# Kernel tuning notes

Hardware: AMD Instinct MI355X
Metric: run time of the kernel (lower is better)

## Reference

```python
import math
import jax, jax.numpy as jnp
import numpy as np

B, S, D, H = 4, 1024, 512, 8
DK = D // H


def lin(x, W, b):
    # torch nn.Linear: y = x @ W.T + b, W: [out, in]
    return jnp.einsum('...i,oi->...o', x, W) + b


def layer_norm(x, scale, bias, eps=1e-5):
    m = jnp.mean(x, axis=-1, keepdims=True)
    v = jnp.var(x, axis=-1, keepdims=True)
    return (x - m) / jnp.sqrt(v + eps) * scale + bias


def mha(q_in, k_in, v_in, Wq, bq, Wk, bk, Wv, bv, Wo, bo, gammas, mask, zero_pad):
    b, s, _ = q_in.shape
    q = lin(q_in, Wq, bq).reshape(b, s, H, DK).transpose(0, 2, 1, 3)  # bhsd
    k = lin(k_in, Wk, bk).reshape(b, s, H, DK).transpose(0, 2, 1, 3)
    v = lin(v_in, Wv, bv).reshape(b, s, H, DK).transpose(0, 2, 1, 3)
    scores = jnp.einsum('bhid,bhjd->bhij', q, k) / math.sqrt(DK)
    # no-grad distance-decay branch
    s_ = jnp.where(mask, scores, jnp.float32(-1e32))
    s_ = jax.nn.softmax(s_, axis=-1) * mask
    distcum = jnp.cumsum(s_, axis=-1)
    disttotal = jnp.sum(s_, axis=-1, keepdims=True)
    idx = jnp.arange(s)
    pos = jnp.abs(idx[None, :] - idx[:, None]).astype(jnp.float32)[None, None]  # |i-j|
    dist = jax.lax.stop_gradient(jnp.sqrt(jnp.clip((disttotal - distcum) * pos, 0.0, None)))
    gamma = -jax.nn.softplus(gammas)[None]  # [1,h,1,1]
    total_effect = jnp.clip(jnp.exp(dist * gamma), 1e-5, 1e5)
    scores = scores * total_effect
    # NOTE: original code calls scores.masked_fill(...) without assignment (no-op);
    # faithfully NOT re-masking before this softmax.
    att = jax.nn.softmax(scores, axis=-1)
    if zero_pad:
        att = att.at[:, :, 0, :].set(0.0)
    out = jnp.einsum('bhij,bhjd->bhid', att, v).transpose(0, 2, 1, 3).reshape(b, s, D)
    return lin(out, Wo, bo)


def setup_inputs() -> dict:
    key = jax.random.key(0)
    ks = jax.random.split(key, 32)
    ki = iter(range(32))

    def w(shape, scale=0.02):
        return jax.random.normal(ks[next(ki)], shape, jnp.float32) * scale

    inp = {
        'q_emb': jax.random.normal(ks[next(ki)], (B, S, D), jnp.float32),
        'qa_emb': jax.random.normal(ks[next(ki)], (B, S, D), jnp.float32),
    }
    for blk in (1, 2, 3):
        inp[f'Wq{blk}'] = w((D, D)); inp[f'bq{blk}'] = jnp.zeros((D,), jnp.float32)
        if blk == 3:
            inp['Wk3'] = w((D, D)); inp['bk3'] = jnp.zeros((D,), jnp.float32)
        inp[f'Wv{blk}'] = w((D, D)); inp[f'bv{blk}'] = jnp.zeros((D,), jnp.float32)
        inp[f'Wo{blk}'] = w((D, D)); inp[f'bo{blk}'] = jnp.zeros((D,), jnp.float32)
        inp[f'g{blk}'] = w((H, 1, 1), 0.5)
        inp[f'ls{blk}'] = jnp.ones((D,), jnp.float32)
        inp[f'lb{blk}'] = jnp.zeros((D,), jnp.float32)
    inp['know'] = jax.random.uniform(ks[next(ki)], (1, 1, D), jnp.float32, -1.0, 1.0)
    inp['Wlk'] = w((D, DK)); inp['b_lk'] = jnp.zeros((D,), jnp.float32)
    inp['Wlv'] = w((D, DK)); inp['b_lv'] = jnp.zeros((D,), jnp.float32)
    return inp


def reference(q_emb, qa_emb,
              Wq1, bq1, Wv1, bv1, Wo1, bo1, g1, ls1, lb1,
              Wq2, bq2, Wv2, bv2, Wo2, bo2, g2, ls2, lb2,
              Wq3, bq3, Wk3, bk3, Wv3, bv3, Wo3, bo3, g3, ls3, lb3,
              know, Wlk, b_lk, Wlv, b_lv):
    b, s, d = q_emb.shape
    ones = jnp.ones((s, s), dtype=bool)
    mask_peek = jnp.tril(ones, k=0)[None, None]   # peek_cur=True
    mask_nopeek = jnp.tril(ones, k=-1)[None, None]  # peek_cur=False

    # block1 / block2 share k and q projections (kq_same=True)
    hq = layer_norm(q_emb + mha(q_emb, q_emb, q_emb, Wq1, bq1, Wq1, bq1,
                                Wv1, bv1, Wo1, bo1, g1, mask_peek, False), ls1, lb1)
    ha = layer_norm(qa_emb + mha(qa_emb, qa_emb, qa_emb, Wq2, bq2, Wq2, bq2,
                                 Wv2, bv2, Wo2, bo2, g2, mask_peek, False), ls2, lb2)
    query = jnp.broadcast_to(know, (b, s, d))
    h = layer_norm(query + mha(query, hq, ha, Wq3, bq3, Wk3, bk3,
                               Wv3, bv3, Wo3, bo3, g3, mask_nopeek, True), ls3, lb3)

    # small multi-head combine
    key_t = jax.nn.sigmoid(lin(query.reshape(b, s, H, DK), Wlk, b_lk))  # [b,s,h,d]
    val_t = jax.nn.sigmoid(lin(h.reshape(b, s, H, DK), Wlv, b_lv))     # [b,s,h,d]
    beta = jnp.einsum('bshd,bsd->bsh', key_t, q_emb)
    alpha = jax.nn.softmax(beta, axis=-1)
    out = jnp.einsum('bsh,bshd->bsd', alpha, val_t)
    return out
```

## Files before the change

kernel.cpp:

```cpp
#include <hip/hip_runtime.h>
#include <math.h>

#define BB 4
#define S 1024
#define D 512
#define H 8
#define DKH 64

#define ATT_LD 1032
#define KS_LD  66

typedef __attribute__((ext_vector_type(8))) short bf16x8;
typedef __attribute__((ext_vector_type(4))) float f32x4;

__device__ __forceinline__ unsigned short f2bf(float f){
  unsigned int u = __float_as_uint(f);
  u += 0x7FFFu + ((u >> 16) & 1u);
  return (unsigned short)(u >> 16);
}
__device__ __forceinline__ float bf2f(unsigned int v){
  return __uint_as_float(v << 16);
}
__device__ __forceinline__ f32x4 MFMA(bf16x8 a, bf16x8 b, f32x4 c){
  return __builtin_amdgcn_mfma_f32_16x16x32_bf16(a, b, c, 0, 0, 0);
}
__device__ __forceinline__ void gl_lds16(const void* g, void* l){
  __builtin_amdgcn_global_load_lds(
      (const __attribute__((address_space(1))) void*)g,
      (__attribute__((address_space(3))) void*)l, 16, 0, 0);
}

__device__ __forceinline__ float blk_sum(float* r, int t, float v){
  r[t] = v; __syncthreads();
  for (int s = 128; s > 0; s >>= 1){
    if (t < s) r[t] += r[t + s];
    __syncthreads();
  }
  float res = r[0]; __syncthreads();
  return res;
}

struct GemmJobs {
  const unsigned short* A[4];
  const unsigned short* W[4];
  const float* bias[4];
  void* C[4];
};
template<int OUTBF>
__global__ __launch_bounds__(256) void mfma_gemm_b(GemmJobs jb)
{
  __shared__ __align__(16) short As[128][32];
  __shared__ __align__(16) short Ws[128][32];
  const int t = threadIdx.x;
  const int z = blockIdx.z;
  const int n0 = blockIdx.x * 128, m0 = blockIdx.y * 128;
  const unsigned short* A = jb.A[z];
  const unsigned short* W = jb.W[z];
  const float* bias = jb.bias[z];
  const int w = t >> 6, lane = t & 63;
  const int wm = (w >> 1) << 6, wn = (w & 1) << 6;
  const int lm = lane & 15, q = lane >> 4;
  const int r = t >> 2, cc = (t & 3) << 3;
  char* ldsA = ((char*)&As[0][0]) + w * 1024;
  char* ldsW = ((char*)&Ws[0][0]) + w * 1024;
  f32x4 acc[4][4];
  #pragma unroll
  for (int a_ = 0; a_ < 4; a_++)
    #pragma unroll
    for (int b_ = 0; b_ < 4; b_++)
      acc[a_][b_] = (f32x4){0.f, 0.f, 0.f, 0.f};
  for (int k0 = 0; k0 < D; k0 += 32){
    gl_lds16(&A[(size_t)(m0 + r)      * D + k0 + cc], ldsA);
    gl_lds16(&A[(size_t)(m0 + r + 64) * D + k0 + cc], ldsA + 4096);
    gl_lds16(&W[(size_t)(n0 + r)      * D + k0 + cc], ldsW);
    gl_lds16(&W[(size_t)(n0 + r + 64) * D + k0 + cc], ldsW + 4096);
    __syncthreads();
    bf16x8 af[4], bf[4];
    #pragma unroll
    for (int mt = 0; mt < 4; mt++) af[mt] = *(const bf16x8*)&As[wm + mt*16 + lm][q*8];
    #pragma unroll
    for (int nt = 0; nt < 4; nt++) bf[nt] = *(const bf16x8*)&Ws[wn + nt*16 + lm][q*8];
    #pragma unroll
    for (int mt = 0; mt < 4; mt++)
      #pragma unroll
      for (int nt = 0; nt < 4; nt++)
        acc[mt][nt] = MFMA(af[mt], bf[nt], acc[mt][nt]);
    __syncthreads();
  }
  #pragma unroll
  for (int nt = 0; nt < 4; nt++){
    const int n = n0 + wn + nt*16 + lm;
    const float bs = bias[n];
    #pragma unroll
    for (int mt = 0; mt < 4; mt++){
      const int mb = m0 + wm + mt*16 + (q << 2);
      f32x4 c = acc[mt][nt];
      #pragma unroll
      for (int rr = 0; rr < 4; rr++){
        float vv = c[rr] + bs;
        if (OUTBF)
          ((unsigned short*)jb.C[z])[(size_t)(mb + rr) * D + n] = f2bf(vv);
        else
          ((float*)jb.C[z])[(size_t)(mb + rr) * D + n] = vv;
      }
    }
  }
}

struct VTArgs { const unsigned short* v[2]; unsigned short* vt[2]; };
__global__ __launch_bounds__(256) void vt_kernel(VTArgs a)
{
  __shared__ unsigned short tile[64 * KS_LD];
  const int z = blockIdx.z, bh = blockIdx.y, b = bh >> 3, h = bh & 7;
  const int j0 = blockIdx.x * 64;
  const int t = threadIdx.x;
  const unsigned short* vp = a.v[z];
  unsigned short* vtp = a.vt[z] + (size_t)bh * 64 * S;
  #pragma unroll
  for (int p = 0; p < 2; p++){
    int lin = t + p * 256, row = lin >> 3, c8 = (lin & 7) << 3;
    *(uint4*)&tile[row * KS_LD + c8] =
      *(const uint4*)&vp[((size_t)b * S + j0 + row) * D + h * DKH + c8];
  }
  __syncthreads();
  #pragma unroll
  for (int p = 0; p < 2; p++){
    int lin = t + p * 256, d = lin >> 3, c8 = (lin & 7) << 3;
    unsigned short tmp[8];
    #pragma unroll
    for (int jx = 0; jx < 8; jx++) tmp[jx] = tile[(c8 + jx) * KS_LD + d];
    *(uint4*)&vtp[(size_t)d * S + j0 + c8] = *(const uint4*)tmp;
  }
}

struct FAArgs {
  const unsigned short* qk[2];
  const unsigned short* vt[2];
  unsigned short* ctx[2];
  const float* g[2];
  const float* c3;
  int diag, zero_pad;
};
template<int C3>
__global__ __launch_bounds__(256) void fused_attn(FAArgs a)
{
  __shared__ __align__(16) unsigned short att[32 * ATT_LD];
  __shared__ __align__(16) unsigned short Ks[64 * KS_LD];
  const int t = threadIdx.x;
  const int z = blockIdx.z;
  const int bh = blockIdx.y, b = bh >> 3, h = bh & 7;
  const int i0 = blockIdx.x * 32;
  const int w = t >> 6, lane = t & 63, lm = lane & 15, q = lane >> 4;
  const unsigned short* qkp = a.qk[z];
  const unsigned short* vtp = a.vt[z] + (size_t)bh * 64 * S;
  unsigned short* ctxp = a.ctx[z];
  const int r0 = t >> 3, c8 = (t & 7) << 3;
  float gm;
  { float gv = a.g[z][h]; gm = -((gv > 20.f) ? gv : log1pf(expf(gv))); }

  if (!C3){
    bf16x8 af[2][2];
    #pragma unroll
    for (int mt = 0; mt < 2; mt++)
      #pragma unroll
      for (int kft = 0; kft < 2; kft++)
        af[mt][kft] = *(const bf16x8*)
          &qkp[((size_t)b * S + i0 + mt*16 + lm) * D + h * DKH + kft*32 + q*8];
    uint4 k0v = *(const uint4*)&qkp[((size_t)b * S + r0)      * D + h * DKH + c8];
    uint4 k1v = *(const uint4*)&qkp[((size_t)b * S + r0 + 32) * D + h * DKH + c8];
    for (int jc = 0; jc < S; jc += 64){
      *(uint4*)&Ks[r0 * KS_LD + c8]        = k0v;
      *(uint4*)&Ks[(r0 + 32) * KS_LD + c8] = k1v;
      __syncthreads();
      if (jc + 64 < S){
        k0v = *(const uint4*)&qkp[((size_t)b * S + jc + 64 + r0)      * D + h * DKH + c8];
        k1v = *(const uint4*)&qkp[((size_t)b * S + jc + 64 + r0 + 32) * D + h * DKH + c8];
      }
      bf16x8 bv0 = *(const bf16x8*)&Ks[(w*16 + lm) * KS_LD + q*8];
      bf16x8 bv1 = *(const bf16x8*)&Ks[(w*16 + lm) * KS_LD + 32 + q*8];
      #pragma unroll
      for (int mt = 0; mt < 2; mt++){
        f32x4 acc = (f32x4){0.f, 0.f, 0.f, 0.f};
        acc = MFMA(af[mt][0], bv0, acc);
        acc = MFMA(af[mt][1], bv1, acc);
        #pragma unroll
        for (int rr = 0; rr < 4; rr++)
          att[(mt*16 + q*4 + rr) * ATT_LD + jc + w*16 + lm] = f2bf(acc[rr] * 0.125f);
      }
      __syncthreads();
    }
  }

  uint4 v0 = *(const uint4*)&vtp[(size_t)r0 * S + c8];
  uint4 v1 = *(const uint4*)&vtp[(size_t)(r0 + 32) * S + c8];

  const int jA0 = lane * 8, jB0 = 512 + lane * 8;
  for (int rloc = 0; rloc < 8; rloc++){
    const int i = i0 + w*8 + rloc;
    unsigned short* rowp = &att[(w*8 + rloc) * ATT_LD];
    if (C3 && a.zero_pad && i == 0){
      uint4 zz = make_uint4(0u,0u,0u,0u);
      *(uint4*)&rowp[jA0] = zz;
      *(uint4*)&rowp[jB0] = zz;
      continue;
    }
    float c[16];
    if (C3){
      const float* c3p = a.c3 + ((size_t)b * H + h) * S;
      #pragma unroll
      for (int sg = 0; sg < 2; sg++)
        #pragma unroll
        for (int p4 = 0; p4 < 2; p4++){
          float4 x = *(const float4*)&c3p[sg*512 + lane*8 + p4*4];
          c[sg*8+p4*4+0] = x.x; c[sg*8+p4*4+1] = x.y;
          c[sg*8+p4*4+2] = x.z; c[sg*8+p4*4+3] = x.w;
        }
    } else {
      #pragma unroll
      for (int sg = 0; sg < 2; sg++){
        uint4 u = *(const uint4*)&rowp[sg*512 + lane*8];
        unsigned int uu[4] = {u.x, u.y, u.z, u.w};
        #pragma unroll
        for (int mel = 0; mel < 4; mel++){
          c[sg*8 + mel*2]     = bf2f(uu[mel] & 0xffffu);
          c[sg*8 + mel*2 + 1] = bf2f(uu[mel] >> 16);
        }
      }
    }
    const int jmax = i + a.diag;
    float pl[16];
    float runA = 0.f, runB = 0.f;
    #pragma unroll
    for (int k = 0; k < 8; k++){
      float e = (jA0 + k <= jmax) ? __expf(c[k]) : 0.f;
      runA += e; pl[k] = runA;
    }
    #pragma unroll
    for (int k = 0; k < 8; k++){
      float e = (jB0 + k <= jmax) ? __expf(c[8+k]) : 0.f;
      runB += e; pl[8+k] = runB;
    }
    float sA = runA, sB = runB;
    #pragma unroll
    for (int off = 1; off < 64; off <<= 1){
      float uA = __shfl_up(sA, off, 64);
      float uB = __shfl_up(sB, off, 64);
      if (lane >= off){ sA += uA; sB += uB; }
    }
    const float TA = __shfl(sA, 63, 64);
    const float T  = TA + __shfl(sB, 63, 64);
    const float inv1 = 1.f / T;
    const float cbaseA = (T - (sA - runA)) * inv1;
    const float cbaseB = (T - (TA + sB - runB)) * inv1;
    const float fiA = (float)(i - jA0);
    const float fiB = (float)(i - jB0);
    float ls2 = 0.f;
    #pragma unroll
    for (int k = 0; k < 8; k++){
      float remn = fmaf(-pl[k], inv1, cbaseA);
      float pos  = fabsf(fiA - (float)k);
      float dist = sqrtf(fmaxf(remn * pos, 0.f));
      float eff  = fmaxf(__expf(gm * dist), 1e-5f);
      float pp   = __expf(c[k] * eff);
      ls2 += pp; pl[k] = pp;
    }
    #pragma unroll
    for (int k = 0; k < 8; k++){
      float remn = fmaf(-pl[8+k], inv1, cbaseB);
      float pos  = fabsf(fiB - (float)k);
      float dist = sqrtf(fmaxf(remn * pos, 0.f));
      float eff  = fmaxf(__expf(gm * dist), 1e-5f);
      float pp   = __expf(c[8+k] * eff);
      ls2 += pp; pl[8+k] = pp;
    }
    #pragma unroll
    for (int off = 1; off < 64; off <<= 1) ls2 += __shfl_xor(ls2, off, 64);
    const float inv2 = 1.f / ls2;
    #pragma unroll
    for (int sg = 0; sg < 2; sg++){
      unsigned int ou[4];
      #pragma unroll
      for (int mel = 0; mel < 4; mel++){
        unsigned int lo = f2bf(pl[sg*8 + 2*mel]     * inv2);
        unsigned int hi = f2bf(pl[sg*8 + 2*mel + 1] * inv2);
        ou[mel] = lo | (hi << 16);
      }
      *(uint4*)&rowp[sg*512 + lane*8] = make_uint4(ou[0], ou[1], ou[2], ou[3]);
    }
  }
  __syncthreads();

  const int mloc = w & 1, nh = w >> 1;
  f32x4 acc0 = (f32x4){0.f,0.f,0.f,0.f};
  f32x4 acc1 = (f32x4){0.f,0.f,0.f,0.f};
  for (int kc = 0; kc < S; kc += 64){
    *(uint4*)&Ks[r0 * KS_LD + c8]        = v0;
    *(uint4*)&Ks[(r0 + 32) * KS_LD + c8] = v1;
    __syncthreads();
    if (kc + 64 < S){
      v0 = *(const uint4*)&vtp[(size_t)r0 * S + kc + 64 + c8];
      v1 = *(const uint4*)&vtp[(size_t)(r0 + 32) * S + kc + 64 + c8];
    }
    #pragma unroll
    for (int kft = 0; kft < 2; kft++){
      bf16x8 afv = *(const bf16x8*)&att[(mloc*16 + lm) * ATT_LD + kc + kft*32 + q*8];
      bf16x8 b0 = *(const bf16x8*)&Ks[((nh*2 + 0)*16 + lm) * KS_LD + kft*32 + q*8];
      bf16x8 b1 = *(const bf16x8*)&Ks[((nh*2 + 1)*16 + lm) * KS_LD + kft*32 + q*8];
      acc0 = MFMA(afv, b0, acc0);
      acc1 = MFMA(afv, b1, acc1);
    }
    __syncthreads();
  }
  #pragma unroll
  for (int nt2 = 0; nt2 < 2; nt2++){
    f32x4 acc = nt2 ? acc1 : acc0;
    const int d = (nh*2 + nt2)*16 + lm;
    #pragma unroll
    for (int rr = 0; rr < 4; rr++){
      const int row = i0 + mloc*16 + q*4 + rr;
      ctxp[((size_t)b * S + row) * D + h * DKH + d] = f2bf(acc[rr]);
    }
  }
}

__global__ __launch_bounds__(256) void ln_residual(
    const float* __restrict__ resid, const float* __restrict__ y,
    const float* __restrict__ ls, const float* __restrict__ lb,
    unsigned short* __restrict__ out, int bcast)
{
  const int r = blockIdx.x, t = threadIdx.x;
  __shared__ float red[256];
  const size_t base = (size_t)r * D;
  float r0 = bcast ? resid[t]       : resid[base + t];
  float r1 = bcast ? resid[t + 256] : resid[base + t + 256];
  float x0 = r0 + y[base + t];
  float x1 = r1 + y[base + t + 256];
  float mean = blk_sum(red, t, x0 + x1) * (1.0f / 512.0f);
  float d0 = x0 - mean, d1 = x1 - mean;
  float var = blk_sum(red, t, d0*d0 + d1*d1) * (1.0f / 512.0f);
  float inv = rsqrtf(var + 1e-5f);
  out[base + t]       = f2bf(d0 * inv * ls[t]       + lb[t]);
  out[base + t + 256] = f2bf(d1 * inv * ls[t + 256] + lb[t + 256]);
}

struct CvtJobs {
  const float* s[12];
  unsigned short* d[12];
  int n[12];
};
__global__ __launch_bounds__(256) void cvt_all(CvtJobs jb){
  const int z = blockIdx.y;
  const int n = jb.n[z];
  const float* s = jb.s[z];
  unsigned short* d = jb.d[z];
  for (int idx = blockIdx.x * 256 + threadIdx.x; idx < n; idx += gridDim.x * 256)
    d[idx] = f2bf(s[idx]);
}

__global__ __launch_bounds__(256) void qvec3_kernel(
    const float* __restrict__ know, const float* __restrict__ Wq3,
    const float* __restrict__ bq3, float* __restrict__ q3)
{
  int n = blockIdx.x * 256 + threadIdx.x;
  float acc = 0.f;
  for (int d = 0; d < 512; d++) acc += know[d] * Wq3[(size_t)n * 512 + d];
  q3[n] = acc + bq3[n];
}

__global__ __launch_bounds__(256) void keyt_kernel(
    const float* __restrict__ know, const float* __restrict__ Wlk,
    const float* __restrict__ blk_, float* __restrict__ keyt)
{
  int idx = blockIdx.x * 256 + threadIdx.x;
  int h = idx >> 9, n = idx & 511;
  float acc = 0.f;
  for (int i = 0; i < 64; i++) acc += know[h * 64 + i] * Wlk[(size_t)n * 64 + i];
  keyt[idx] = 1.f / (1.f + __expf(-(acc + blk_[n])));
}

__global__ __launch_bounds__(256) void scores3_kernel(
    const float* __restrict__ q3, const unsigned short* __restrict__ k3,
    float* __restrict__ c3)
{
  int idx = blockIdx.x * 256 + threadIdx.x;
  int j  = idx & (S - 1);
  int bh = idx >> 10;
  int h  = bh & 7, b = bh >> 3;
  const unsigned short* kp = k3 + ((size_t)b * S + j) * D + h * DKH;
  const float* qp = q3 + h * DKH;
  float acc = 0.f;
  #pragma unroll
  for (int d8 = 0; d8 < 64; d8 += 8){
    uint4 u = *(const uint4*)&kp[d8];
    unsigned int uu[4] = {u.x, u.y, u.z, u.w};
    #pragma unroll
    for (int mel = 0; mel < 4; mel++){
      acc += qp[d8 + 2*mel]     * bf2f(uu[mel] & 0xffffu);
      acc += qp[d8 + 2*mel + 1] * bf2f(uu[mel] >> 16);
    }
  }
  c3[idx] = acc * 0.125f;
}

__global__ __launch_bounds__(256) void alphas_kernel(
    const float* __restrict__ keyt, const float* __restrict__ q_emb,
    float* __restrict__ alpha)
{
  const int row = blockIdx.x * 4 + (threadIdx.x >> 6);
  const int l = threadIdx.x & 63;
  const int h = l >> 3, sub = l & 7;
  const float* qr = q_emb + (size_t)row * D;
  const float* kt = keyt + h * D;
  float p = 0.f;
  for (int d = sub; d < D; d += 8) p += kt[d] * qr[d];
  p += __shfl_xor(p, 1, 64);
  p += __shfl_xor(p, 2, 64);
  p += __shfl_xor(p, 4, 64);
  float m = p;
  m = fmaxf(m, __shfl_xor(m, 8, 64));
  m = fmaxf(m, __shfl_xor(m, 16, 64));
  m = fmaxf(m, __shfl_xor(m, 32, 64));
  float e = __expf(p - m);
  float ssum = e;
  ssum += __shfl_xor(ssum, 8, 64);
  ssum += __shfl_xor(ssum, 16, 64);
  ssum += __shfl_xor(ssum, 32, 64);
  if (sub == 0) alpha[(size_t)row * H + h] = e / ssum;
}

__global__ __launch_bounds__(256) void val_fused(
    const unsigned short* __restrict__ Ah,
    const unsigned short* __restrict__ Wv,
    const float* __restrict__ blv,
    const float* __restrict__ alpha,
    float* __restrict__ out)
{
  __shared__ __align__(16) short As[128][32];
  __shared__ __align__(16) short Ws[128][32];
  __shared__ float als[128];
  const int t = threadIdx.x;
  const int n0 = blockIdx.x * 128, m0 = blockIdx.y * 128;
  if (t < 128) als[t] = alpha[m0 + t];
  const int w = t >> 6, lane = t & 63;
  const int wm = (w >> 1) << 6, wn = (w & 1) << 6;
  const int lm = lane & 15, q = lane >> 4;
  const int r = t >> 2, cc = (t & 3) << 3;
  f32x4 acc[4][4];
  #pragma unroll
  for (int a_ = 0; a_ < 4; a_++)
    #pragma unroll
    for (int b_ = 0; b_ < 4; b_++)
      acc[a_][b_] = (f32x4){0.f, 0.f, 0.f, 0.f};
  for (int k0 = 0; k0 < 64; k0 += 32){
    *(uint4*)&As[r][cc]      = *(const uint4*)&Ah[(size_t)(m0 + r) * 64 + k0 + cc];
    *(uint4*)&As[r + 64][cc] = *(const uint4*)&Ah[(size_t)(m0 + r + 64) * 64 + k0 + cc];
    *(uint4*)&Ws[r][cc]      = *(const uint4*)&Wv[(size_t)(n0 + r) * 64 + k0 + cc];
    *(uint4*)&Ws[r + 64][cc] = *(const uint4*)&Wv[(size_t)(n0 + r + 64) * 64 + k0 + cc];
    __syncthreads();
    bf16x8 af[4], bf[4];
    #pragma unroll
    for (int mt = 0; mt < 4; mt++) af[mt] = *(const bf16x8*)&As[wm + mt*16 + lm][q*8];
    #pragma unroll
    for (int nt = 0; nt < 4; nt++) bf[nt] = *(const bf16x8*)&Ws[wn + nt*16 + lm][q*8];
    #pragma unroll
    for (int mt = 0; mt < 4; mt++)
      #pragma unroll
      for (int nt = 0; nt < 4; nt++)
        acc[mt][nt] = MFMA(af[mt], bf[nt], acc[mt][nt]);
    __syncthreads();
  }
  #pragma unroll
  for (int nt = 0; nt < 4; nt++){
    const int n = n0 + wn + nt*16 + lm;
    const float bs = blv[n];
    #pragma unroll
    for (int mt = 0; mt < 4; mt++){
      const int mb = m0 + wm + mt*16;
      f32x4 c = acc[mt][nt];
      float part = 0.f;
      #pragma unroll
      for (int rr = 0; rr < 4; rr++){
        const int ml = (mb - m0) + (q << 2) + rr;
        float sg = 1.f / (1.f + __expf(-(c[rr] + bs)));
        part += als[ml] * sg;
      }
      part += __shfl_xor(part, 16, 64);
      if ((q & 1) == 0){
        const int srow = (mb >> 3) + (q >> 1);
        out[(size_t)srow * D + n] = part;
      }
    }
  }
}

extern "C" void kernel_launch(void* const* d_in, const int* in_sizes, int n_in,
                              void* d_out, int out_size, void* d_ws, size_t ws_size,
                              hipStream_t stream) {
  const float* q_emb  = (const float*)d_in[0];
  const float* qa_emb = (const float*)d_in[1];
  const float* Wq1 = (const float*)d_in[2],  *bq1 = (const float*)d_in[3];
  const float* Wv1 = (const float*)d_in[4],  *bv1 = (const float*)d_in[5];
  const float* Wo1 = (const float*)d_in[6],  *bo1 = (const float*)d_in[7];
  const float* g1  = (const float*)d_in[8],  *ls1 = (const float*)d_in[9],  *lb1 = (const float*)d_in[10];
  const float* Wq2 = (const float*)d_in[11], *bq2 = (const float*)d_in[12];
  const float* Wv2 = (const float*)d_in[13], *bv2 = (const float*)d_in[14];
  const float* Wo2 = (const float*)d_in[15], *bo2 = (const float*)d_in[16];
  const float* g2  = (const float*)d_in[17], *ls2 = (const float*)d_in[18], *lb2 = (const float*)d_in[19];
  const float* Wq3 = (const float*)d_in[20], *bq3 = (const float*)d_in[21];
  const float* Wk3 = (const float*)d_in[22], *bk3 = (const float*)d_in[23];
  const float* Wv3 = (const float*)d_in[24], *bv3 = (const float*)d_in[25];
  const float* Wo3 = (const float*)d_in[26], *bo3 = (const float*)d_in[27];
  const float* g3  = (const float*)d_in[28], *ls3 = (const float*)d_in[29], *lb3 = (const float*)d_in[30];
  const float* know = (const float*)d_in[31];
  const float* Wlk  = (const float*)d_in[32], *b_lk = (const float*)d_in[33];
  const float* Wlv  = (const float*)d_in[34], *b_lv = (const float*)d_in[35];
  float* outp = (float*)d_out;

  const size_t NSD = (size_t)BB * S * D;
  unsigned short* p = (unsigned short*)d_ws;
  unsigned short* qk1b = p; p += NSD;
  unsigned short* v1b  = p; p += NSD;
  unsigned short* qk2b = p; p += NSD;
  unsigned short* v2b  = p; p += NSD;
  unsigned short* k3b  = p; p += NSD;
  unsigned short* v3b  = p; p += NSD;
  unsigned short* ctx1b= p; p += NSD;
  unsigned short* ctx2b= p; p += NSD;
  unsigned short* ctx3b= p; p += NSD;
  unsigned short* xqb  = p; p += NSD;
  unsigned short* xab  = p; p += NSD;
  unsigned short* hqb  = p; p += NSD;
  unsigned short* hab  = p; p += NSD;
  unsigned short* hfb  = p; p += NSD;
  unsigned short* vt1  = p; p += NSD;
  unsigned short* vt2  = p; p += NSD;
  unsigned short* vt3  = p; p += NSD;
  unsigned short* wb   = p; p += (size_t)9 * D * D;
  unsigned short* wlvb = p; p += (size_t)D * DKH;
  float* yv0   = (float*)p;
  float* yv1   = yv0 + NSD;
  float* q3    = yv1 + NSD;
  float* keyt  = q3 + 512;
  float* c3    = keyt + 4096;
  float* alpha = c3 + (size_t)BB * H * S;

  unsigned short* Wq1b = wb + 0*(size_t)D*D;
  unsigned short* Wv1b = wb + 1*(size_t)D*D;
  unsigned short* Wo1b = wb + 2*(size_t)D*D;
  unsigned short* Wq2b = wb + 3*(size_t)D*D;
  unsigned short* Wv2b = wb + 4*(size_t)D*D;
  unsigned short* Wo2b = wb + 5*(size_t)D*D;
  unsigned short* Wk3b = wb + 6*(size_t)D*D;
  unsigned short* Wv3b = wb + 7*(size_t)D*D;
  unsigned short* Wo3b = wb + 8*(size_t)D*D;

  CvtJobs jb;
  jb.s[0] = q_emb;  jb.d[0] = xqb;  jb.n[0] = (int)NSD;
  jb.s[1] = qa_emb; jb.d[1] = xab;  jb.n[1] = (int)NSD;
  jb.s[2] = Wq1; jb.d[2] = Wq1b; jb.n[2] = D*D;
  jb.s[3] = Wv1; jb.d[3] = Wv1b; jb.n[3] = D*D;
  jb.s[4] = Wo1; jb.d[4] = Wo1b; jb.n[4] = D*D;
  jb.s[5] = Wq2; jb.d[5] = Wq2b; jb.n[5] = D*D;
  jb.s[6] = Wv2; jb.d[6] = Wv2b; jb.n[6] = D*D;
  jb.s[7] = Wo2; jb.d[7] = Wo2b; jb.n[7] = D*D;
  jb.s[8] = Wk3; jb.d[8] = Wk3b; jb.n[8] = D*D;
  jb.s[9] = Wv3; jb.d[9] = Wv3b; jb.n[9] = D*D;
  jb.s[10] = Wo3; jb.d[10] = Wo3b; jb.n[10] = D*D;
  jb.s[11] = Wlv; jb.d[11] = wlvb; jb.n[11] = D*DKH;
  cvt_all<<<dim3(256, 12), 256, 0, stream>>>(jb);

  {
    GemmJobs g;
    g.A[0]=xqb; g.W[0]=Wq1b; g.bias[0]=bq1; g.C[0]=qk1b;
    g.A[1]=xqb; g.W[1]=Wv1b; g.bias[1]=bv1; g.C[1]=v1b;
    g.A[2]=xab; g.W[2]=Wq2b; g.bias[2]=bq2; g.C[2]=qk2b;
    g.A[3]=xab; g.W[3]=Wv2b; g.bias[3]=bv2; g.C[3]=v2b;
    mfma_gemm_b<1><<<dim3(4, 32, 4), 256, 0, stream>>>(g);
  }
  { VTArgs a; a.v[0]=v1b; a.v[1]=v2b; a.vt[0]=vt1; a.vt[1]=vt2;
    vt_kernel<<<dim3(16, 32, 2), 256, 0, stream>>>(a); }
  { FAArgs a;
    a.qk[0]=qk1b; a.qk[1]=qk2b; a.vt[0]=vt1; a.vt[1]=vt2;
    a.ctx[0]=ctx1b; a.ctx[1]=ctx2b; a.g[0]=g1; a.g[1]=g2;
    a.c3=nullptr; a.diag=0; a.zero_pad=0;
    fused_attn<0><<<dim3(32, 32, 2), 256, 0, stream>>>(a); }
  {
    GemmJobs g;
    g.A[0]=ctx1b; g.W[0]=Wo1b; g.bias[0]=bo1; g.C[0]=yv0;
    g.A[1]=ctx2b; g.W[1]=Wo2b; g.bias[1]=bo2; g.C[1]=yv1;
    g.A[2]=ctx1b; g.W[2]=Wo1b; g.bias[2]=bo1; g.C[2]=yv0;
    g.A[3]=ctx1b; g.W[3]=Wo1b; g.bias[3]=bo1; g.C[3]=yv0;
    mfma_gemm_b<0><<<dim3(4, 32, 2), 256, 0, stream>>>(g);
  }
  ln_residual<<<BB*S, 256, 0, stream>>>(q_emb,  yv0, ls1, lb1, hqb, 0);
  ln_residual<<<BB*S, 256, 0, stream>>>(qa_emb, yv1, ls2, lb2, hab, 0);

  qvec3_kernel<<<2, 256, 0, stream>>>(know, Wq3, bq3, q3);
  {
    GemmJobs g;
    g.A[0]=hqb; g.W[0]=Wk3b; g.bias[0]=bk3; g.C[0]=k3b;
    g.A[1]=hab; g.W[1]=Wv3b; g.bias[1]=bv3; g.C[1]=v3b;
    g.A[2]=hqb; g.W[2]=Wk3b; g.bias[2]=bk3; g.C[2]=k3b;
    g.A[3]=hqb; g.W[3]=Wk3b; g.bias[3]=bk3; g.C[3]=k3b;
    mfma_gemm_b<1><<<dim3(4, 32, 2), 256, 0, stream>>>(g);
  }
  { VTArgs a; a.v[0]=v3b; a.v[1]=v3b; a.vt[0]=vt3; a.vt[1]=vt3;
    vt_kernel<<<dim3(16, 32, 1), 256, 0, stream>>>(a); }
  scores3_kernel<<<128, 256, 0, stream>>>(q3, k3b, c3);
  { FAArgs a;
    a.qk[0]=k3b; a.qk[1]=k3b; a.vt[0]=vt3; a.vt[1]=vt3;
    a.ctx[0]=ctx3b; a.ctx[1]=ctx3b; a.g[0]=g3; a.g[1]=g3;
    a.c3=c3; a.diag=-1; a.zero_pad=1;
    fused_attn<1><<<dim3(32, 32, 1), 256, 0, stream>>>(a); }
  {
    GemmJobs g;
    g.A[0]=ctx3b; g.W[0]=Wo3b; g.bias[0]=bo3; g.C[0]=yv0;
    g.A[1]=ctx3b; g.W[1]=Wo3b; g.bias[1]=bo3; g.C[1]=yv0;
    g.A[2]=ctx3b; g.W[2]=Wo3b; g.bias[2]=bo3; g.C[2]=yv0;
    g.A[3]=ctx3b; g.W[3]=Wo3b; g.bias[3]=bo3; g.C[3]=yv0;
    mfma_gemm_b<0><<<dim3(4, 32, 1), 256, 0, stream>>>(g);
  }
  ln_residual<<<BB*S, 256, 0, stream>>>(know, yv0, ls3, lb3, hfb, 1);

  keyt_kernel<<<16, 256, 0, stream>>>(know, Wlk, b_lk, keyt);
  alphas_kernel<<<1024, 256, 0, stream>>>(keyt, q_emb, alpha);
  val_fused<<<dim3(4, 256), 256, 0, stream>>>(hfb, wlvb, b_lv, alpha, outp);
}
```

Before: 482.4 us.

## Halve attention row tile, drop K/V LDS staging, use exp2, wave-parallel qvec3

The fused attention kernel now handles 16 query rows per block instead of 32, which doubles the grid and halves the LDS score buffer so more blocks fit per CU. K and V^T fragments are read straight from global memory rather than staged through shared memory, removing the per-chunk __syncthreads barriers. The softmax and decay exponentials are rewritten in base 2 with pre-scaled LOG2E inputs. The qvec3 GEMV now uses one wave per output with vectorized loads and a shuffle reduction instead of one thread per output. The trade-off is more redundant global and L2 traffic for K/V, since each block loads them without LDS reuse.

```diff
diff --git a/kernel.cpp b/kernel.cpp
--- a/kernel.cpp
+++ b/kernel.cpp
@@ -8,7 +8,7 @@
 #define DKH 64
 
 #define ATT_LD 1032
-#define KS_LD  66
+#define LOG2E 1.4426950408889634f
 
 typedef __attribute__((ext_vector_type(8))) short bf16x8;
 typedef __attribute__((ext_vector_type(4))) float f32x4;
@@ -107,6 +107,7 @@
   }
 }
 
+#define KS_LD 66
 struct VTArgs { const unsigned short* v[2]; unsigned short* vt[2]; };
 __global__ __launch_bounds__(256) void vt_kernel(VTArgs a)
 {
@@ -144,60 +145,41 @@
 template<int C3>
 __global__ __launch_bounds__(256) void fused_attn(FAArgs a)
 {
-  __shared__ __align__(16) unsigned short att[32 * ATT_LD];
-  __shared__ __align__(16) unsigned short Ks[64 * KS_LD];
+  __shared__ __align__(16) unsigned short att[16 * ATT_LD];
   const int t = threadIdx.x;
   const int z = blockIdx.z;
   const int bh = blockIdx.y, b = bh >> 3, h = bh & 7;
-  const int i0 = blockIdx.x * 32;
+  const int i0 = blockIdx.x * 16;
   const int w = t >> 6, lane = t & 63, lm = lane & 15, q = lane >> 4;
   const unsigned short* qkp = a.qk[z];
   const unsigned short* vtp = a.vt[z] + (size_t)bh * 64 * S;
   unsigned short* ctxp = a.ctx[z];
-  const int r0 = t >> 3, c8 = (t & 7) << 3;
-  float gm;
-  { float gv = a.g[z][h]; gm = -((gv > 20.f) ? gv : log1pf(expf(gv))); }
+  float gm2;
+  { float gv = a.g[z][h];
+    gm2 = -((gv > 20.f) ? gv : log1pf(expf(gv))) * LOG2E; }
 
   if (!C3){
-    bf16x8 af[2][2];
-    #pragma unroll
-    for (int mt = 0; mt < 2; mt++)
-      #pragma unroll
-      for (int kft = 0; kft < 2; kft++)
-        af[mt][kft] = *(const bf16x8*)
-          &qkp[((size_t)b * S + i0 + mt*16 + lm) * D + h * DKH + kft*32 + q*8];
-    uint4 k0v = *(const uint4*)&qkp[((size_t)b * S + r0)      * D + h * DKH + c8];
-    uint4 k1v = *(const uint4*)&qkp[((size_t)b * S + r0 + 32) * D + h * DKH + c8];
+    bf16x8 af0 = *(const bf16x8*)&qkp[((size_t)b * S + i0 + lm) * D + h * DKH + q*8];
+    bf16x8 af1 = *(const bf16x8*)&qkp[((size_t)b * S + i0 + lm) * D + h * DKH + 32 + q*8];
     for (int jc = 0; jc < S; jc += 64){
-      *(uint4*)&Ks[r0 * KS_LD + c8]        = k0v;
-      *(uint4*)&Ks[(r0 + 32) * KS_LD + c8] = k1v;
-      __syncthreads();
-      if (jc + 64 < S){
-        k0v = *(const uint4*)&qkp[((size_t)b * S + jc + 64 + r0)      * D + h * DKH + c8];
-        k1v = *(const uint4*)&qkp[((size_t)b * S + jc + 64 + r0 + 32) * D + h * DKH + c8];
-      }
-      bf16x8 bv0 = *(const bf16x8*)&Ks[(w*16 + lm) * KS_LD + q*8];
-      bf16x8 bv1 = *(const bf16x8*)&Ks[(w*16 + lm) * KS_LD + 32 + q*8];
-      #pragma unroll
-      for (int mt = 0; mt < 2; mt++){
-        f32x4 acc = (f32x4){0.f, 0.f, 0.f, 0.f};
-        acc = MFMA(af[mt][0], bv0, acc);
-        acc = MFMA(af[mt][1], bv1, acc);
-        #pragma unroll
-        for (int rr = 0; rr < 4; rr++)
-          att[(mt*16 + q*4 + rr) * ATT_LD + jc + w*16 + lm] = f2bf(acc[rr] * 0.125f);
-      }
-      __syncthreads();
-    }
-  }
-
-  uint4 v0 = *(const uint4*)&vtp[(size_t)r0 * S + c8];
-  uint4 v1 = *(const uint4*)&vtp[(size_t)(r0 + 32) * S + c8];
+      const int jrow = jc + w*16 + lm;
+      const size_t kb = ((size_t)b * S + jrow) * D + h * DKH;
+      bf16x8 bv0 = *(const bf16x8*)&qkp[kb + q*8];
+      bf16x8 bv1 = *(const bf16x8*)&qkp[kb + 32 + q*8];
+      f32x4 acc = (f32x4){0.f, 0.f, 0.f, 0.f};
+      acc = MFMA(af0, bv0, acc);
+      acc = MFMA(af1, bv1, acc);
+      #pragma unroll
+      for (int rr = 0; rr < 4; rr++)
+        att[(q*4 + rr) * ATT_LD + jc + w*16 + lm] = f2bf(acc[rr] * 0.125f);
+    }
+  }
+  __syncthreads();
 
   const int jA0 = lane * 8, jB0 = 512 + lane * 8;
-  for (int rloc = 0; rloc < 8; rloc++){
-    const int i = i0 + w*8 + rloc;
-    unsigned short* rowp = &att[(w*8 + rloc) * ATT_LD];
+  for (int rloc = 0; rloc < 4; rloc++){
+    const int i = i0 + w*4 + rloc;
+    unsigned short* rowp = &att[(w*4 + rloc) * ATT_LD];
     if (C3 && a.zero_pad && i == 0){
       uint4 zz = make_uint4(0u,0u,0u,0u);
       *(uint4*)&rowp[jA0] = zz;
@@ -212,8 +194,8 @@
         #pragma unroll
         for (int p4 = 0; p4 < 2; p4++){
           float4 x = *(const float4*)&c3p[sg*512 + lane*8 + p4*4];
-          c[sg*8+p4*4+0] = x.x; c[sg*8+p4*4+1] = x.y;
-          c[sg*8+p4*4+2] = x.z; c[sg*8+p4*4+3] = x.w;
+          c[sg*8+p4*4+0] = x.x * LOG2E; c[sg*8+p4*4+1] = x.y * LOG2E;
+          c[sg*8+p4*4+2] = x.z * LOG2E; c[sg*8+p4*4+3] = x.w * LOG2E;
         }
     } else {
       #pragma unroll
@@ -222,8 +204,8 @@
         unsigned int uu[4] = {u.x, u.y, u.z, u.w};
         #pragma unroll
         for (int mel = 0; mel < 4; mel++){
-          c[sg*8 + mel*2]     = bf2f(uu[mel] & 0xffffu);
-          c[sg*8 + mel*2 + 1] = bf2f(uu[mel] >> 16);
+          c[sg*8 + mel*2]     = bf2f(uu[mel] & 0xffffu) * LOG2E;
+          c[sg*8 + mel*2 + 1] = bf2f(uu[mel] >> 16) * LOG2E;
         }
       }
     }
@@ -232,12 +214,12 @@
     float runA = 0.f, runB = 0.f;
     #pragma unroll
     for (int k = 0; k < 8; k++){
-      float e = (jA0 + k <= jmax) ? __expf(c[k]) : 0.f;
+      float e = (jA0 + k <= jmax) ? exp2f(c[k]) : 0.f;
       runA += e; pl[k] = runA;
     }
     #pragma unroll
     for (int k = 0; k < 8; k++){
-      float e = (jB0 + k <= jmax) ? __expf(c[8+k]) : 0.f;
+      float e = (jB0 + k <= jmax) ? exp2f(c[8+k]) : 0.f;
       runB += e; pl[8+k] = runB;
     }
     float sA = runA, sB = runB;
@@ -260,8 +242,8 @@
       float remn = fmaf(-pl[k], inv1, cbaseA);
       float pos  = fabsf(fiA - (float)k);
       float dist = sqrtf(fmaxf(remn * pos, 0.f));
-      float eff  = fmaxf(__expf(gm * dist), 1e-5f);
-      float pp   = __expf(c[k] * eff);
+      float eff  = fmaxf(exp2f(gm2 * dist), 1e-5f);
+      float pp   = exp2f(c[k] * eff);
       ls2 += pp; pl[k] = pp;
     }
     #pragma unroll
@@ -269,8 +251,8 @@
       float remn = fmaf(-pl[8+k], inv1, cbaseB);
       float pos  = fabsf(fiB - (float)k);
       float dist = sqrtf(fmaxf(remn * pos, 0.f));
-      float eff  = fmaxf(__expf(gm * dist), 1e-5f);
-      float pp   = __expf(c[8+k] * eff);
+      float eff  = fmaxf(exp2f(gm2 * dist), 1e-5f);
+      float pp   = exp2f(c[8+k] * eff);
       ls2 += pp; pl[8+k] = pp;
     }
     #pragma unroll
@@ -290,36 +272,19 @@
   }
   __syncthreads();
 
-  const int mloc = w & 1, nh = w >> 1;
-  f32x4 acc0 = (f32x4){0.f,0.f,0.f,0.f};
-  f32x4 acc1 = (f32x4){0.f,0.f,0.f,0.f};
+  f32x4 acc = (f32x4){0.f,0.f,0.f,0.f};
   for (int kc = 0; kc < S; kc += 64){
-    *(uint4*)&Ks[r0 * KS_LD + c8]        = v0;
-    *(uint4*)&Ks[(r0 + 32) * KS_LD + c8] = v1;
-    __syncthreads();
-    if (kc + 64 < S){
-      v0 = *(const uint4*)&vtp[(size_t)r0 * S + kc + 64 + c8];
-      v1 = *(const uint4*)&vtp[(size_t)(r0 + 32) * S + kc + 64 + c8];
-    }
     #pragma unroll
     for (int kft = 0; kft < 2; kft++){
-      bf16x8 afv = *(const bf16x8*)&att[(mloc*16 + lm) * ATT_LD + kc + kft*32 + q*8];
-      bf16x8 b0 = *(const bf16x8*)&Ks[((nh*2 + 0)*16 + lm) * KS_LD + kft*32 + q*8];
-      bf16x8 b1 = *(const bf16x8*)&Ks[((nh*2 + 1)*16 + lm) * KS_LD + kft*32 + q*8];
-      acc0 = MFMA(afv, b0, acc0);
-      acc1 = MFMA(afv, b1, acc1);
-    }
-    __syncthreads();
-  }
-  #pragma unroll
-  for (int nt2 = 0; nt2 < 2; nt2++){
-    f32x4 acc = nt2 ? acc1 : acc0;
-    const int d = (nh*2 + nt2)*16 + lm;
-    #pragma unroll
-    for (int rr = 0; rr < 4; rr++){
-      const int row = i0 + mloc*16 + q*4 + rr;
-      ctxp[((size_t)b * S + row) * D + h * DKH + d] = f2bf(acc[rr]);
-    }
+      bf16x8 afv = *(const bf16x8*)&att[lm * ATT_LD + kc + kft*32 + q*8];
+      bf16x8 bv  = *(const bf16x8*)&vtp[(size_t)(w*16 + lm) * S + kc + kft*32 + q*8];
+      acc = MFMA(afv, bv, acc);
+    }
+  }
+  #pragma unroll
+  for (int rr = 0; rr < 4; rr++){
+    const int row = i0 + q*4 + rr;
+    ctxp[((size_t)b * S + row) * D + h * DKH + w*16 + lm] = f2bf(acc[rr]);
   }
 }
 
@@ -361,10 +326,17 @@
     const float* __restrict__ know, const float* __restrict__ Wq3,
     const float* __restrict__ bq3, float* __restrict__ q3)
 {
-  int n = blockIdx.x * 256 + threadIdx.x;
-  float acc = 0.f;
-  for (int d = 0; d < 512; d++) acc += know[d] * Wq3[(size_t)n * 512 + d];
-  q3[n] = acc + bq3[n];
+  const int wv = (blockIdx.x * 256 + threadIdx.x) >> 6;
+  const int lane = threadIdx.x & 63;
+  const float* wr = Wq3 + (size_t)wv * 512 + lane * 8;
+  const float* kr = know + lane * 8;
+  float4 w0 = *(const float4*)&wr[0], w1 = *(const float4*)&wr[4];
+  float4 k0 = *(const float4*)&kr[0], k1 = *(const float4*)&kr[4];
+  float p = w0.x*k0.x + w0.y*k0.y + w0.z*k0.z + w0.w*k0.w
+          + w1.x*k1.x + w1.y*k1.y + w1.z*k1.z + w1.w*k1.w;
+  #pragma unroll
+  for (int off = 1; off < 64; off <<= 1) p += __shfl_xor(p, off, 64);
+  if (lane == 0) q3[wv] = p + bq3[wv];
 }
 
 __global__ __launch_bounds__(256) void keyt_kernel(
@@ -583,7 +555,7 @@
     a.qk[0]=qk1b; a.qk[1]=qk2b; a.vt[0]=vt1; a.vt[1]=vt2;
     a.ctx[0]=ctx1b; a.ctx[1]=ctx2b; a.g[0]=g1; a.g[1]=g2;
     a.c3=nullptr; a.diag=0; a.zero_pad=0;
-    fused_attn<0><<<dim3(32, 32, 2), 256, 0, stream>>>(a); }
+    fused_attn<0><<<dim3(64, 32, 2), 256, 0, stream>>>(a); }
   {
     GemmJobs g;
     g.A[0]=ctx1b; g.W[0]=Wo1b; g.bias[0]=bo1; g.C[0]=yv0;
@@ -595,7 +567,7 @@
   ln_residual<<<BB*S, 256, 0, stream>>>(q_emb,  yv0, ls1, lb1, hqb, 0);
   ln_residual<<<BB*S, 256, 0, stream>>>(qa_emb, yv1, ls2, lb2, hab, 0);
 
-  qvec3_kernel<<<2, 256, 0, stream>>>(know, Wq3, bq3, q3);
+  qvec3_kernel<<<128, 256, 0, stream>>>(know, Wq3, bq3, q3);
   {
     GemmJobs g;
     g.A[0]=hqb; g.W[0]=Wk3b; g.bias[0]=bk3; g.C[0]=k3b;
@@ -611,7 +583,7 @@
     a.qk[0]=k3b; a.qk[1]=k3b; a.vt[0]=vt3; a.vt[1]=vt3;
     a.ctx[0]=ctx3b; a.ctx[1]=ctx3b; a.g[0]=g3; a.g[1]=g3;
     a.c3=c3; a.diag=-1; a.zero_pad=1;
-    fused_attn<1><<<dim3(32, 32, 1), 256, 0, stream>>>(a); }
+    fused_attn<1><<<dim3(64, 32, 1), 256, 0, stream>>>(a); }
   {
     GemmJobs g;
     g.A[0]=ctx3b; g.W[0]=Wo3b; g.bias[0]=bo3; g.C[0]=yv0;
```

Result: no change. 478.8 us (-0.7%).
